# Kernel optimization log

Hardware: AMD Instinct MI355X
Metric: run time of the kernel (lower is better)

Reference implementation:

```python
import jax, jax.numpy as jnp
import numpy as np


def _dct_basis(N):
    # X[k] = 2 * sum_n x[n] * cos(pi * k * (2n+1) / (2N))  -- matches the
    # flip+concat+rfft+twiddle path of the torch module (unnormalized DCT-II x2).
    k = jnp.arange(N, dtype=jnp.float32)[:, None]
    n = jnp.arange(N, dtype=jnp.float32)[None, :]
    return 2.0 * jnp.cos(jnp.pi * k * (2.0 * n + 1.0) / (2.0 * N))  # (K, N)


def _dct2(x):
    B, C, H, W = x.shape
    Bw = _dct_basis(W)
    Bh = _dct_basis(H)
    x = jnp.einsum('bchw,kw->bchk', x, Bw)  # DCT along W
    x = jnp.einsum('bchw,kh->bckw', x, Bh)  # DCT along H
    return x


def _conv3x3(x, w, b):
    y = jax.lax.conv_general_dilated(x, w, window_strides=(1, 1), padding='SAME',
                                     dimension_numbers=('NCHW', 'OIHW', 'NCHW'))
    return y + b[None, :, None, None]


def _bn(x, g, be, m, v):
    # inference-mode BatchNorm2d, eps = 1e-5
    inv = jax.lax.rsqrt(v + 1e-5)
    return (x - m[None, :, None, None]) * (g * inv)[None, :, None, None] + be[None, :, None, None]


def setup_inputs() -> dict:
    key = jax.random.key(0)
    ks = jax.random.split(key, 16)
    B, C, H, W = 32, 1, 224, 224
    mid, emb = 128, 256
    s = 0.05
    return {
        'x':  jax.random.normal(ks[0], (B, C, H, W), jnp.float32),
        'w1': jax.random.normal(ks[1], (64, C, 3, 3), jnp.float32) * s,
        'b1': jax.random.normal(ks[2], (64,), jnp.float32) * s,
        'g1': jax.random.uniform(ks[3], (64,), jnp.float32, 0.5, 1.5),
        'be1': jax.random.normal(ks[4], (64,), jnp.float32) * s,
        'm1': jax.random.normal(ks[5], (64,), jnp.float32) * s,
        'v1': jax.random.uniform(ks[6], (64,), jnp.float32, 0.5, 1.5),
        'w2': jax.random.normal(ks[7], (mid, 64, 3, 3), jnp.float32) * s,
        'b2': jax.random.normal(ks[8], (mid,), jnp.float32) * s,
        'g2': jax.random.uniform(ks[9], (mid,), jnp.float32, 0.5, 1.5),
        'be2': jax.random.normal(ks[10], (mid,), jnp.float32) * s,
        'm2': jax.random.normal(ks[11], (mid,), jnp.float32) * s,
        'v2': jax.random.uniform(ks[12], (mid,), jnp.float32, 0.5, 1.5),
        'wp': jax.random.normal(ks[13], (emb, mid), jnp.float32) * s,
        'bp': jax.random.normal(ks[14], (emb,), jnp.float32) * s,
    }


def reference(x, w1, b1, g1, be1, m1, v1, w2, b2, g2, be2, m2, v2, wp, bp):
    USE_TOPK = 0.5
    X = _dct2(x)                                   # (B, 1, H, W)
    B, C, H, W = X.shape
    k_h, k_w = int(H * USE_TOPK), int(W * USE_TOPK)
    mask = jnp.zeros((H, W), X.dtype).at[:k_h, :k_w].set(1.0)
    X = X * mask[None, None]
    h = jax.nn.relu(_bn(_conv3x3(X, w1, b1), g1, be1, m1, v1))
    h = jax.nn.relu(_bn(_conv3x3(h, w2, b2), g2, be2, m2, v2))
    h = jnp.mean(h, axis=(2, 3))                   # AdaptiveAvgPool2d((1,1)) -> (B, mid)
    return h @ wp.T + bp                           # (B, emb_dim)
```

## Files before the change

### kernel.cpp

```cpp
#include <hip/hip_runtime.h>
#include <math.h>


#define NPIX 224
#define KEEP 112
#define H1DIM 115
#define ADIM 114

typedef short bf16x8 __attribute__((ext_vector_type(8)));
typedef float f32x4  __attribute__((ext_vector_type(4)));
typedef float f32x16 __attribute__((ext_vector_type(16)));

__device__ __forceinline__ unsigned short f2bf(float f) {
    unsigned int u = __float_as_uint(f);
    unsigned int r = (u + 0x7FFFu + ((u >> 16) & 1u)) >> 16;
    return (unsigned short)r;
}

__global__ __launch_bounds__(256) void prep_kernel(
    const float* __restrict__ w1, const float* __restrict__ b1,
    const float* __restrict__ g1, const float* __restrict__ be1,
    const float* __restrict__ m1, const float* __restrict__ v1,
    const float* __restrict__ w2,
    float* __restrict__ Bst, float* __restrict__ P,
    float* __restrict__ ws1, float* __restrict__ wb1,
    uint4* __restrict__ w2f) {
    int bx = blockIdx.x, tid = threadIdx.x;
    if (bx < 49) {
        int idx = bx * 256 + tid;
        if (idx < KEEP * KEEP) {
            int n = idx / KEEP, k = idx - n * KEEP;
            double ang = 3.14159265358979323846 * (double)k * (2.0 * n + 1.0) / (2.0 * NPIX);
            Bst[n * KEEP + k] = (float)(2.0 * cos(ang));
        }
    } else if (bx < 54) {
        __shared__ float c1s[64];
        if (tid < 64) {
            float sc = g1[tid] * rsqrtf(v1[tid] + 1e-5f);
            c1s[tid] = fmaxf((b1[tid] - m1[tid]) * sc + be1[tid], 0.f);
        }
        __syncthreads();
        int idx = (bx - 49) * 256 + tid;
        if (idx < 128 * 9) {
            int oc = idx / 9, tap = idx - oc * 9;
            float s = 0.f;
            for (int ic = 0; ic < 64; ++ic)
                s = fmaf(w2[((size_t)oc * 64 + ic) * 9 + tap], c1s[ic], s);
            P[idx] = s;
        }
    } else if (bx == 54) {
        if (tid < 64) {
            float sc = g1[tid] * rsqrtf(v1[tid] + 1e-5f);
            wb1[tid] = (b1[tid] - m1[tid]) * sc + be1[tid];
            for (int t = 0; t < 9; ++t) ws1[tid * 9 + t] = w1[tid * 9 + t] * sc;
        }
    } else {
        int j = (bx - 55) * 256 + tid;
        if (j < 9216) {
            int q = j >> 6, lane = j & 63;
            int tap = q / 16, rem = q & 15;
            int kc = rem >> 2, g32 = rem & 3;
            int oc = g32 * 32 + (lane & 31);
            int ic0 = kc * 16 + (lane >> 5) * 8;
            union { unsigned short us[8]; uint4 v; } u;
#pragma unroll
            for (int t_ = 0; t_ < 8; ++t_)
                u.us[t_] = f2bf(w2[((size_t)oc * 64 + ic0 + t_) * 9 + tap]);
            w2f[j] = u.v;
        }
    }
}

__global__ __launch_bounds__(128) void dct_w_kernel(const float* __restrict__ x,
                                                    const float* __restrict__ Bst,
                                                    float* __restrict__ tmp1) {
    int blk = blockIdx.x;
    int tid = threadIdx.x;
    __shared__ float eo[2][4][112];
    const float* rows = x + (size_t)blk * 4 * NPIX;
    for (int i = tid; i < 448; i += 128) {
        int r = i / 112, n = i - r * 112;
        float a = rows[r * NPIX + n], bv = rows[r * NPIX + 223 - n];
        eo[0][r][n] = a + bv;
        eo[1][r][n] = a - bv;
    }
    __syncthreads();
    int kw = tid;
    if (kw >= KEEP) return;
    const float* eop = &eo[kw & 1][0][0];
    float a0 = 0.f, a1 = 0.f, a2 = 0.f, a3 = 0.f;
    for (int n = 0; n < 112; ++n) {
        float bs = Bst[n * KEEP + kw];
        a0 = fmaf(eop[n], bs, a0);
        a1 = fmaf(eop[112 + n], bs, a1);
        a2 = fmaf(eop[224 + n], bs, a2);
        a3 = fmaf(eop[336 + n], bs, a3);
    }
    size_t base = (size_t)blk * 4 * KEEP + kw;
    tmp1[base] = a0; tmp1[base + 112] = a1; tmp1[base + 224] = a2; tmp1[base + 336] = a3;
}

__global__ __launch_bounds__(512) void dct_h_kernel(const float* __restrict__ tmp1,
                                                    const float* __restrict__ Bst,
                                                    float* __restrict__ Xd) {
    int kq = blockIdx.x, b = blockIdx.y;
    int tid = threadIdx.x;
    int kw = tid & 127, sub = tid >> 7;
    __shared__ float ps[3][4][112];
    const int kh0 = kq * 4;
    float a0 = 0.f, a1 = 0.f, a2 = 0.f, a3 = 0.f;
    if (kw < KEEP) {
        const float* t = tmp1 + (size_t)b * NPIX * KEEP + kw;
        for (int h = sub * 28; h < sub * 28 + 28; ++h) {
            float lo = t[(size_t)h * KEEP];
            float hi = t[(size_t)(223 - h) * KEEP];
            float e = lo + hi, o = lo - hi;
            const float* bs = Bst + h * KEEP + kh0;
            a0 = fmaf(e, bs[0], a0);
            a1 = fmaf(o, bs[1], a1);
            a2 = fmaf(e, bs[2], a2);
            a3 = fmaf(o, bs[3], a3);
        }
        if (sub) {
            ps[sub - 1][0][kw] = a0; ps[sub - 1][1][kw] = a1;
            ps[sub - 1][2][kw] = a2; ps[sub - 1][3][kw] = a3;
        }
    }
    __syncthreads();
    if (sub == 0 && kw < KEEP) {
        a0 += ps[0][0][kw] + ps[1][0][kw] + ps[2][0][kw];
        a1 += ps[0][1][kw] + ps[1][1][kw] + ps[2][1][kw];
        a2 += ps[0][2][kw] + ps[1][2][kw] + ps[2][2][kw];
        a3 += ps[0][3][kw] + ps[1][3][kw] + ps[2][3][kw];
        float* X = Xd + ((size_t)b * KEEP + kh0) * KEEP + kw;
        X[0] = a0; X[112] = a1; X[224] = a2; X[336] = a3;
    }
}

__global__ __launch_bounds__(256) void conv1_kernel(const float* __restrict__ Xd,
                                                    const float* __restrict__ ws1,
                                                    const float* __restrict__ wb1,
                                                    unsigned short* __restrict__ h1c) {
    const int r = blockIdx.y, b = blockIdx.z;
    const int c0 = blockIdx.x * 32;
    const int tid = threadIdx.x;
    __shared__ float xs[3][36];
    __shared__ float wsm[8][73];
    __shared__ float wbs[64];
    const float* X = Xd + (size_t)b * KEEP * KEEP;
    for (int i = tid; i < 102; i += 256) {
        int dr = i / 34, dc = i - dr * 34;
        int rr = r - 1 + dr, cc = c0 - 1 + dc;
        xs[dr][dc] = ((unsigned)rr < (unsigned)KEEP && (unsigned)cc < (unsigned)KEEP)
                         ? X[rr * KEEP + cc] : 0.f;
    }
    for (int i = tid; i < 576; i += 256) {
        int ic = i / 9, t = i - ic * 9;
        wsm[ic >> 3][(ic & 7) * 9 + t] = ws1[i];
    }
    if (tid < 64) wbs[tid] = wb1[tid];
    __syncthreads();

    const int px = tid >> 3, icg = tid & 7;
    const int c = c0 + px;
    float xv[9];
#pragma unroll
    for (int ky = 0; ky < 3; ++ky)
#pragma unroll
        for (int kx = 0; kx < 3; ++kx) xv[ky * 3 + kx] = xs[ky][px + kx];

    union { unsigned short us[8]; uint4 v; } u;
#pragma unroll
    for (int j = 0; j < 8; ++j) {
        float s = wbs[icg * 8 + j];
#pragma unroll
        for (int t = 0; t < 9; ++t) s = fmaf(xv[t], wsm[icg][j * 9 + t], s);
        u.us[j] = f2bf(fmaxf(s, 0.f));
    }
    if (c < H1DIM) {
        unsigned short* dst = h1c + (((size_t)b * H1DIM + r) * H1DIM + c) * 64 + icg * 8;
        *reinterpret_cast<uint4*>(dst) = u.v;
    }
}

__global__ __launch_bounds__(512, 4) void conv2_mfma_kernel(
    const unsigned short* __restrict__ h1c, const uint4* __restrict__ w2f,
    const float* __restrict__ b2, const float* __restrict__ g2,
    const float* __restrict__ be2, const float* __restrict__ m2,
    const float* __restrict__ v2, float* __restrict__ partial) {
    const int tc = blockIdx.x, tr = blockIdx.y, b = blockIdx.z;
    const int r0 = tr * 16, c0 = tc * 16;
    const int tid = threadIdx.x;
    const int lane = tid & 63, w = tid >> 6;
    const int mg = w & 3, og = w >> 2;

    __shared__ unsigned short At[324 * 64];

    const unsigned short* __restrict__ h1b = h1c + (size_t)b * (H1DIM * H1DIM * 64);
    for (int e = tid; e < 2592; e += 512) {
        int px = e >> 3, gi = e & 7;
        int pr = px / 18, pc = px - pr * 18;
        int gr = r0 + pr - 1, gc = c0 + pc - 1;
        uint4 v = make_uint4(0u, 0u, 0u, 0u);
        if ((unsigned)gr < (unsigned)H1DIM && (unsigned)gc < (unsigned)H1DIM)
            v = *reinterpret_cast<const uint4*>(h1b + ((size_t)(gr * H1DIM + gc)) * 64 + gi * 8);
        *reinterpret_cast<uint4*>(&At[px * 64 + ((gi * 8) ^ ((px & 7) << 3))]) = v;
    }
    __syncthreads();

    f32x16 acc[2][2];
#pragma unroll
    for (int F = 0; F < 2; ++F)
#pragma unroll
        for (int N = 0; N < 2; ++N)
#pragma unroll
            for (int i = 0; i < 16; ++i) acc[F][N][i] = 0.f;

    const int flim2 = ADIM - r0 - 4 * mg;
    if (flim2 > 0) {
        const int rowbase = 4 * mg + ((lane & 31) >> 4);
        const int colbase = lane & 15;
        const int khalf = (lane >> 5) * 8;
#pragma unroll
        for (int s = 0; s < 36; ++s) {
            const int tap = s >> 2, kc = s & 3;
            const int ky = tap / 3, kx = tap - 3 * ky;
            const int icoff = kc * 16 + khalf;
            const bf16x8* bq = reinterpret_cast<const bf16x8*>(
                w2f + (size_t)(((tap * 4 + kc) * 4) + og * 2) * 64 + lane);
            const bf16x8 b0 = bq[0];
            const bf16x8 b1 = bq[64];
#pragma unroll
            for (int F = 0; F < 2; ++F) {
                if (2 * F < flim2) {
                    const int px = (rowbase + 2 * F + ky) * 18 + colbase + kx;
                    const bf16x8 a = *reinterpret_cast<const bf16x8*>(
                        &At[px * 64 + (icoff ^ ((px & 7) << 3))]);
                    acc[F][0] = __builtin_amdgcn_mfma_f32_32x32x16_bf16(a, b0, acc[F][0], 0, 0, 0);
                    acc[F][1] = __builtin_amdgcn_mfma_f32_32x32x16_bf16(a, b1, acc[F][1], 0, 0, 0);
                }
            }
        }
    }

    const int tile = tr * 8 + tc;
    float* pslice = partial + (((size_t)b * 64 + tile) * 4 + mg) * 128;
#pragma unroll
    for (int N = 0; N < 2; ++N) {
        int oc = og * 64 + N * 32 + (lane & 31);
        float sc = g2[oc] * rsqrtf(v2[oc] + 1e-5f);
        float bias = b2[oc] - m2[oc];
        float add = be2[oc];
        float s = 0.f;
#pragma unroll
        for (int F = 0; F < 2; ++F) {
#pragma unroll
            for (int rg = 0; rg < 16; ++rg) {
                int m = (rg & 3) + 8 * (rg >> 2) + 4 * (lane >> 5);
                int p = ((2 * mg + F) << 5) + m;
                int row = r0 + (p >> 4);
                int col = c0 + (p & 15);
                float v = fmaxf(fmaf(acc[F][N][rg] + bias, sc, add), 0.f);
                s += (row < ADIM && col < ADIM) ? v : 0.f;
            }
        }
        s += __shfl_xor(s, 32);
        if (lane < 32) pslice[og * 64 + N * 32 + lane] = s;
    }
}

__global__ __launch_bounds__(256) void reduce_mean_kernel(
    const float* __restrict__ partial, const float* __restrict__ P,
    const float* __restrict__ b2, const float* __restrict__ g2,
    const float* __restrict__ be2, const float* __restrict__ m2,
    const float* __restrict__ v2, float* __restrict__ mean) {
    int b = blockIdx.x, ocg = blockIdx.y;
    int tid = threadIdx.x;
    int ocl = tid & 15, jq = tid >> 4;
    int oc = ocg * 16 + ocl;
    const float* pb = partial + (size_t)b * 256 * 128 + oc;
    float s = 0.f;
#pragma unroll
    for (int jj = 0; jj < 16; ++jj) s += pb[(size_t)(jq * 16 + jj) * 128];
    __shared__ float red[16][17];
    red[jq][ocl] = s;
    __syncthreads();
    if (jq == 0) {
        float tot = 0.f;
#pragma unroll
        for (int k = 0; k < 16; ++k) tot += red[k][ocl];

        float p[9];
#pragma unroll
        for (int t = 0; t < 9; ++t) p[t] = P[oc * 9 + t];

        float Sall = p[0] + p[1] + p[2] + p[3] + p[4] + p[5] + p[6] + p[7] + p[8];
        float Stop = p[3] + p[4] + p[5] + p[6] + p[7] + p[8];
        float Sbot = p[0] + p[1] + p[2] + p[3] + p[4] + p[5];
        float Sleft  = p[1] + p[2] + p[4] + p[5] + p[7] + p[8];
        float Sright = p[0] + p[1] + p[3] + p[4] + p[6] + p[7];
        float Ctr = p[3] + p[4] + p[6] + p[7];
        float Cbl = p[1] + p[2] + p[4] + p[5];
        float Cbr = p[0] + p[1] + p[3] + p[4];

        float bias = b2[oc], mm = m2[oc], bb = be2[oc];
        float sc = g2[oc] * rsqrtf(v2[oc] + 1e-5f);
#define VALOF(S) fmaxf(((bias) + (S) - (mm)) * (sc) + (bb), 0.f)
        float cs = 36515.f * VALOF(Sall) + 109.f * VALOF(Stop) + 109.f * VALOF(Sleft)
                 + 222.f * VALOF(Sbot) + 222.f * VALOF(Sright)
                 + VALOF(Ctr) + VALOF(Cbl) + VALOF(Cbr);
#undef VALOF
        mean[b * 128 + oc] = (tot + cs) * (1.f / (224.f * 224.f));
    }
}

__global__ __launch_bounds__(256) void final_linear_kernel(const float* __restrict__ mean,
                                                           const float* __restrict__ wp,
                                                           const float* __restrict__ bp,
                                                           float* __restrict__ out) {
    int b = blockIdx.x, e = threadIdx.x;
    __shared__ float mrow[128];
    if (threadIdx.x < 128) mrow[threadIdx.x] = mean[b * 128 + threadIdx.x];
    __syncthreads();
    const float4* wr = reinterpret_cast<const float4*>(wp + (size_t)e * 128);
    float s = bp[e];
#pragma unroll 8
    for (int c = 0; c < 32; ++c) {
        float4 wv = wr[c];
        s = fmaf(mrow[4 * c], wv.x, s);
        s = fmaf(mrow[4 * c + 1], wv.y, s);
        s = fmaf(mrow[4 * c + 2], wv.z, s);
        s = fmaf(mrow[4 * c + 3], wv.w, s);
    }
    out[(size_t)b * 256 + e] = s;
}

extern "C" void kernel_launch(void* const* d_in, const int* in_sizes, int n_in,
                              void* d_out, int out_size, void* d_ws, size_t ws_size,
                              hipStream_t stream) {
    const float* x   = (const float*)d_in[0];
    const float* w1  = (const float*)d_in[1];
    const float* b1  = (const float*)d_in[2];
    const float* g1  = (const float*)d_in[3];
    const float* be1 = (const float*)d_in[4];
    const float* m1  = (const float*)d_in[5];
    const float* v1  = (const float*)d_in[6];
    const float* w2  = (const float*)d_in[7];
    const float* b2  = (const float*)d_in[8];
    const float* g2  = (const float*)d_in[9];
    const float* be2 = (const float*)d_in[10];
    const float* m2  = (const float*)d_in[11];
    const float* v2  = (const float*)d_in[12];
    const float* wp  = (const float*)d_in[13];
    const float* bp  = (const float*)d_in[14];
    float* out = (float*)d_out;

    float* ws = (float*)d_ws;
    size_t off = 0;
    float* Bst  = ws + off; off += (size_t)KEEP * KEEP;
    float* tmp1 = ws + off; off += (size_t)32 * NPIX * KEEP;
    float* Xd   = ws + off; off += (size_t)32 * KEEP * KEEP;
    float* P    = ws + off; off += 128 * 9;
    float* ws1  = ws + off; off += 64 * 9;
    float* wb1  = ws + off; off += 64;
    uint4* w2f  = (uint4*)(ws + off); off += (size_t)9216 * 4;
    float* part = ws + off; off += (size_t)32 * 256 * 128;
    float* mean = ws + off; off += 32 * 128;
    unsigned short* h1c = (unsigned short*)(ws + off);
    off += (size_t)32 * H1DIM * H1DIM * 64 / 2;

    if (ws_size < off * sizeof(float)) return;

    prep_kernel<<<dim3(91), dim3(256), 0, stream>>>(w1, b1, g1, be1, m1, v1, w2,
                                                    Bst, P, ws1, wb1, w2f);
    dct_w_kernel<<<dim3(32 * 56), dim3(128), 0, stream>>>(x, Bst, tmp1);
    dct_h_kernel<<<dim3(28, 32), dim3(512), 0, stream>>>(tmp1, Bst, Xd);
    conv1_kernel<<<dim3(4, H1DIM, 32), dim3(256), 0, stream>>>(Xd, ws1, wb1, h1c);
    conv2_mfma_kernel<<<dim3(8, 8, 32), dim3(512), 0, stream>>>(
        h1c, w2f, b2, g2, be2, m2, v2, part);
    reduce_mean_kernel<<<dim3(32, 8), dim3(256), 0, stream>>>(part, P, b2, g2, be2, m2, v2, mean);
    final_linear_kernel<<<dim3(32), dim3(256), 0, stream>>>(mean, wp, bp, out);
}
```

Before: 135.9 us.

## Remap conv1 to one pixel per thread and restructure conv2 LDS addressing

conv1 now assigns one output pixel per thread over a flattened pixel grid and computes all 64 channels, staging results in a swizzled LDS tile so global stores stay coalesced. This replaces the old layout of 8 threads per pixel with tiny per-row blocks, cutting block count and redundant halo loads. conv2 gets a new LDS swizzle with LDS addresses precomputed per tap, plus a branch-free fast path for full tiles. Weights are read straight from global memory in conv1 rather than LDS, which may add load pressure.

After: 125.1 us. -8.0%, faster.

```diff
diff --git a/kernel.cpp b/kernel.cpp
--- a/kernel.cpp
+++ b/kernel.cpp
@@ -5,6 +5,7 @@
 #define NPIX 224
 #define KEEP 112
 #define H1DIM 115
+#define NPX1 (H1DIM * H1DIM)
 #define ADIM 114
 
 typedef short bf16x8 __attribute__((ext_vector_type(8)));
@@ -141,45 +142,49 @@
                                                     const float* __restrict__ ws1,
                                                     const float* __restrict__ wb1,
                                                     unsigned short* __restrict__ h1c) {
-    const int r = blockIdx.y, b = blockIdx.z;
-    const int c0 = blockIdx.x * 32;
+    const int b = blockIdx.y;
+    const int p0 = blockIdx.x * 256;
     const int tid = threadIdx.x;
-    __shared__ float xs[3][36];
-    __shared__ float wsm[8][73];
-    __shared__ float wbs[64];
+    const int p = p0 + tid;
+    __shared__ uint4 Lt[2048];
+
+    const bool valid = p < NPX1;
+    int r = p / H1DIM, c = p - r * H1DIM;
     const float* X = Xd + (size_t)b * KEEP * KEEP;
-    for (int i = tid; i < 102; i += 256) {
-        int dr = i / 34, dc = i - dr * 34;
-        int rr = r - 1 + dr, cc = c0 - 1 + dc;
-        xs[dr][dc] = ((unsigned)rr < (unsigned)KEEP && (unsigned)cc < (unsigned)KEEP)
-                         ? X[rr * KEEP + cc] : 0.f;
-    }
-    for (int i = tid; i < 576; i += 256) {
-        int ic = i / 9, t = i - ic * 9;
-        wsm[ic >> 3][(ic & 7) * 9 + t] = ws1[i];
-    }
-    if (tid < 64) wbs[tid] = wb1[tid];
-    __syncthreads();
-
-    const int px = tid >> 3, icg = tid & 7;
-    const int c = c0 + px;
     float xv[9];
 #pragma unroll
     for (int ky = 0; ky < 3; ++ky)
 #pragma unroll
-        for (int kx = 0; kx < 3; ++kx) xv[ky * 3 + kx] = xs[ky][px + kx];
-
-    union { unsigned short us[8]; uint4 v; } u;
-#pragma unroll
-    for (int j = 0; j < 8; ++j) {
-        float s = wbs[icg * 8 + j];
-#pragma unroll
-        for (int t = 0; t < 9; ++t) s = fmaf(xv[t], wsm[icg][j * 9 + t], s);
-        u.us[j] = f2bf(fmaxf(s, 0.f));
-    }
-    if (c < H1DIM) {
-        unsigned short* dst = h1c + (((size_t)b * H1DIM + r) * H1DIM + c) * 64 + icg * 8;
-        *reinterpret_cast<uint4*>(dst) = u.v;
+        for (int kx = 0; kx < 3; ++kx) {
+            int rr = r + ky - 1, cc = c + kx - 1;
+            xv[ky * 3 + kx] =
+                (valid && (unsigned)rr < (unsigned)KEEP && (unsigned)cc < (unsigned)KEEP)
+                    ? X[rr * KEEP + cc] : 0.f;
+        }
+
+#pragma unroll 1
+    for (int icg = 0; icg < 8; ++icg) {
+        union { unsigned short us[8]; uint4 v; } u;
+#pragma unroll
+        for (int j = 0; j < 8; ++j) {
+            int ic = icg * 8 + j;
+            float s = wb1[ic];
+#pragma unroll
+            for (int t = 0; t < 9; ++t) s = fmaf(xv[t], ws1[ic * 9 + t], s);
+            u.us[j] = f2bf(fmaxf(s, 0.f));
+        }
+        Lt[tid * 8 + (icg ^ (tid & 7))] = u.v;
+    }
+    __syncthreads();
+
+#pragma unroll
+    for (int k = 0; k < 8; ++k) {
+        int q = k * 256 + tid;
+        int pxl = q >> 3, ig = q & 7;
+        uint4 v = Lt[pxl * 8 + (ig ^ (pxl & 7))];
+        int pg = p0 + pxl;
+        if (pg < NPX1)
+            *reinterpret_cast<uint4*>(h1c + ((size_t)b * NPX1 + pg) * 64 + ig * 8) = v;
     }
 }
 
@@ -196,7 +201,8 @@
 
     __shared__ unsigned short At[324 * 64];
 
-    const unsigned short* __restrict__ h1b = h1c + (size_t)b * (H1DIM * H1DIM * 64);
+    const unsigned short* __restrict__ h1b = h1c + (size_t)b * (NPX1 * 64);
+    char* Atw = reinterpret_cast<char*>(At);
     for (int e = tid; e < 2592; e += 512) {
         int px = e >> 3, gi = e & 7;
         int pr = px / 18, pc = px - pr * 18;
@@ -204,7 +210,8 @@
         uint4 v = make_uint4(0u, 0u, 0u, 0u);
         if ((unsigned)gr < (unsigned)H1DIM && (unsigned)gc < (unsigned)H1DIM)
             v = *reinterpret_cast<const uint4*>(h1b + ((size_t)(gr * H1DIM + gc)) * 64 + gi * 8);
-        *reinterpret_cast<uint4*>(&At[px * 64 + ((gi * 8) ^ ((px & 7) << 3))]) = v;
+        int off = px * 128 + 32 * ((gi >> 1) ^ (px & 3)) + 16 * ((gi & 1) ^ ((px >> 2) & 1));
+        *reinterpret_cast<uint4*>(Atw + off) = v;
     }
     __syncthreads();
 
@@ -217,29 +224,52 @@
             for (int i = 0; i < 16; ++i) acc[F][N][i] = 0.f;
 
     const int flim2 = ADIM - r0 - 4 * mg;
-    if (flim2 > 0) {
-        const int rowbase = 4 * mg + ((lane & 31) >> 4);
-        const int colbase = lane & 15;
-        const int khalf = (lane >> 5) * 8;
+    int A0[9];
+    {
+        const int prb = 4 * mg + ((lane & 31) >> 4);
+        const int cb = lane & 15;
+        const int hb = lane >> 5;
+#pragma unroll
+        for (int ky = 0; ky < 3; ++ky)
+#pragma unroll
+            for (int kx = 0; kx < 3; ++kx) {
+                int px = (prb + ky) * 18 + cb + kx;
+                A0[ky * 3 + kx] = px * 128 + 32 * (px & 3) + 16 * (hb ^ ((px >> 2) & 1));
+            }
+    }
+    const char* Atc = reinterpret_cast<const char*>(At);
+
+    if (flim2 >= 4) {
 #pragma unroll
         for (int s = 0; s < 36; ++s) {
             const int tap = s >> 2, kc = s & 3;
             const int ky = tap / 3, kx = tap - 3 * ky;
-            const int icoff = kc * 16 + khalf;
             const bf16x8* bq = reinterpret_cast<const bf16x8*>(
                 w2f + (size_t)(((tap * 4 + kc) * 4) + og * 2) * 64 + lane);
             const bf16x8 b0 = bq[0];
             const bf16x8 b1 = bq[64];
-#pragma unroll
-            for (int F = 0; F < 2; ++F) {
-                if (2 * F < flim2) {
-                    const int px = (rowbase + 2 * F + ky) * 18 + colbase + kx;
-                    const bf16x8 a = *reinterpret_cast<const bf16x8*>(
-                        &At[px * 64 + (icoff ^ ((px & 7) << 3))]);
-                    acc[F][0] = __builtin_amdgcn_mfma_f32_32x32x16_bf16(a, b0, acc[F][0], 0, 0, 0);
-                    acc[F][1] = __builtin_amdgcn_mfma_f32_32x32x16_bf16(a, b1, acc[F][1], 0, 0, 0);
-                }
-            }
+            const int a0 = A0[ky * 3 + kx] ^ (kc << 5);
+            const int a1 = (a0 ^ 16) + 4608;
+            const bf16x8 va0 = *reinterpret_cast<const bf16x8*>(Atc + a0);
+            const bf16x8 va1 = *reinterpret_cast<const bf16x8*>(Atc + a1);
+            acc[0][0] = __builtin_amdgcn_mfma_f32_32x32x16_bf16(va0, b0, acc[0][0], 0, 0, 0);
+            acc[0][1] = __builtin_amdgcn_mfma_f32_32x32x16_bf16(va0, b1, acc[0][1], 0, 0, 0);
+            acc[1][0] = __builtin_amdgcn_mfma_f32_32x32x16_bf16(va1, b0, acc[1][0], 0, 0, 0);
+            acc[1][1] = __builtin_amdgcn_mfma_f32_32x32x16_bf16(va1, b1, acc[1][1], 0, 0, 0);
+        }
+    } else if (flim2 > 0) {
+#pragma unroll
+        for (int s = 0; s < 36; ++s) {
+            const int tap = s >> 2, kc = s & 3;
+            const int ky = tap / 3, kx = tap - 3 * ky;
+            const bf16x8* bq = reinterpret_cast<const bf16x8*>(
+                w2f + (size_t)(((tap * 4 + kc) * 4) + og * 2) * 64 + lane);
+            const bf16x8 b0 = bq[0];
+            const bf16x8 b1 = bq[64];
+            const int a0 = A0[ky * 3 + kx] ^ (kc << 5);
+            const bf16x8 va0 = *reinterpret_cast<const bf16x8*>(Atc + a0);
+            acc[0][0] = __builtin_amdgcn_mfma_f32_32x32x16_bf16(va0, b0, acc[0][0], 0, 0, 0);
+            acc[0][1] = __builtin_amdgcn_mfma_f32_32x32x16_bf16(va0, b1, acc[0][1], 0, 0, 0);
         }
     }
 
@@ -367,7 +397,7 @@
     float* part = ws + off; off += (size_t)32 * 256 * 128;
     float* mean = ws + off; off += 32 * 128;
     unsigned short* h1c = (unsigned short*)(ws + off);
-    off += (size_t)32 * H1DIM * H1DIM * 64 / 2;
+    off += (size_t)32 * NPX1 * 64 / 2;
 
     if (ws_size < off * sizeof(float)) return;
 
@@ -375,7 +405,7 @@
                                                     Bst, P, ws1, wb1, w2f);
     dct_w_kernel<<<dim3(32 * 56), dim3(128), 0, stream>>>(x, Bst, tmp1);
     dct_h_kernel<<<dim3(28, 32), dim3(512), 0, stream>>>(tmp1, Bst, Xd);
-    conv1_kernel<<<dim3(4, H1DIM, 32), dim3(256), 0, stream>>>(Xd, ws1, wb1, h1c);
+    conv1_kernel<<<dim3(52, 32), dim3(256), 0, stream>>>(Xd, ws1, wb1, h1c);
     conv2_mfma_kernel<<<dim3(8, 8, 32), dim3(512), 0, stream>>>(
         h1c, w2f, b2, g2, be2, m2, v2, part);
     reduce_mean_kernel<<<dim3(32, 8), dim3(256), 0, stream>>>(part, P, b2, g2, be2, m2, v2, mean);
```
